# Kernel tuning notes

Measured on AMD Instinct MI355X. Metric: run time of the kernel, lower is better.

## Reference

```python
import jax
import jax.numpy as jnp
from jax import lax
import numpy as np

SLIDING_WINDOW_LEN = 192
EPS = 1e-6


def setup_inputs() -> dict:
    key = jax.random.key(0)
    X = jax.random.normal(key, (8, 8, 257, 2000), dtype=jnp.float32)
    return {"X": X, "ref_channel": 0}


def _forgetting_normalization(XrMag):
    # XrMag: [B, 1, F, T] magnitude of reference channel
    alpha = (SLIDING_WINDOW_LEN - 1) / (SLIDING_WINDOW_LEN + 1)
    # mean over frequency, keepdim -> [B, 1, 1, T]
    XrMM = XrMag.mean(axis=2, keepdims=True)
    T = XrMM.shape[-1]
    t = jnp.arange(T, dtype=XrMM.dtype)
    # original: alpha_this = min((t-1)/(t+1), alpha) for t < L, else alpha;
    # since (t-1)/(t+1) >= alpha for t >= L, a single minimum is exact.
    a = jnp.minimum((t - 1.0) / (t + 1.0), alpha)  # [T]

    x_seq = jnp.moveaxis(XrMM, -1, 0)  # [T, B, 1, 1]
    mu0 = jnp.zeros_like(x_seq[0])

    def step(mu, inp):
        a_t, x_t = inp
        mu = a_t * mu + (1.0 - a_t) * x_t
        return mu, mu

    _, mus = lax.scan(step, mu0, (a, x_seq))  # [T, B, 1, 1]
    return jnp.moveaxis(mus, 0, -1)  # [B, 1, 1, T]


def reference(X, ref_channel):
    # X: [B, C, F, T] (real stand-in for complex); ref_channel: python int
    Xr = X[:, ref_channel:ref_channel + 1]  # [B, 1, F, T]
    XrMag = jnp.abs(Xr)
    # original detaches XrMM (.detach().cpu()) -> stop_gradient
    XrMM = lax.stop_gradient(_forgetting_normalization(XrMag)) + EPS  # [B,1,1,T]
    X_norm = X / XrMM  # broadcast over C, F
    return X_norm
```

## Files before the change

kernel.cpp:

```cpp
#include <hip/hip_runtime.h>

#define B_N 8
#define C_N 8
#define F_N 257
#define T_N 2000
#define TQ_N (T_N / 4)
#define EPSF 1e-6f

#define FCH 32
#define FPC 9
#define PER_B (C_N * F_N * TQ_N)

#define NBPB   256
#define NTHR_C 256
#define CSTRIDE (NBPB * NTHR_C)
#define CDT     (CSTRIDE % TQ_N)

typedef float f32x4 __attribute__((ext_vector_type(4)));

__global__ __launch_bounds__(512) void partial_mean_kernel(
    const float* __restrict__ X, const int* __restrict__ ref_ch,
    f32x4* __restrict__ part4 )
{
    const int b = blockIdx.x, c = blockIdx.y, tid = threadIdx.x;
    if (tid >= TQ_N) return;

    const int rc = ref_ch[0];
    const f32x4* Xb4 =
        (const f32x4*)(X + ((size_t)(b * C_N + rc)) * (size_t)F_N * T_N);

    const int f0 = c * FPC;
    const int f1 = (f0 + FPC < F_N) ? (f0 + FPC) : F_N;

    f32x4 acc = {0.f, 0.f, 0.f, 0.f};
    for (int f = f0; f < f1; ++f) {
        f32x4 v = Xb4[f * TQ_N + tid];
        acc.x += fabsf(v.x); acc.y += fabsf(v.y);
        acc.z += fabsf(v.z); acc.w += fabsf(v.w);
    }
    part4[(b * FCH + c) * TQ_N + tid] = acc;
}

__global__ __launch_bounds__(512) void scan_kernel(
    const f32x4* __restrict__ part4,
    f32x4* __restrict__ inv4 )
{
    __shared__ float s_mean[T_N];
    __shared__ float s_wA[8];
    __shared__ float s_wB[8];
    const float ALPHA = (float)(191.0 / 193.0);
    const int b = blockIdx.x, tid = threadIdx.x;

    if (tid < TQ_N) {
        f32x4 s = {0.f, 0.f, 0.f, 0.f};
        #pragma unroll
        for (int c = 0; c < FCH; ++c)
            s += part4[(b * FCH + c) * TQ_N + tid];
        const int t = tid * 4;
        const float inv_f = 1.f / (float)F_N;
        s_mean[t + 0] = s.x * inv_f; s_mean[t + 1] = s.y * inv_f;
        s_mean[t + 2] = s.z * inv_f; s_mean[t + 3] = s.w * inv_f;
    }
    __syncthreads();

    float A = 1.f, Bv = 0.f;
    const int tbase = tid * 4;
    #pragma unroll
    for (int k = 0; k < 4; ++k) {
        const int t = tbase + k;
        if (t < T_N) {
            const float tf = (float)t;
            const float a = fminf((tf - 1.f) / (tf + 1.f), ALPHA);
            Bv = a * Bv + (1.f - a) * s_mean[t];
            A  = a * A;
        }
    }
    const int lane = tid & 63;
    #pragma unroll
    for (int d = 1; d < 64; d <<= 1) {
        const float pA = __shfl_up(A, d);
        const float pB = __shfl_up(Bv, d);
        if (lane >= d) { Bv = A * pB + Bv; A = A * pA; }
    }
    const int wid = tid >> 6;
    if (lane == 63) { s_wA[wid] = A; s_wB[wid] = Bv; }
    __syncthreads();
    if (tid == 0) {
        float cA = 1.f, cB = 0.f;
        #pragma unroll
        for (int w = 0; w < 8; ++w) {
            const float nA = s_wA[w] * cA;
            const float nB = s_wA[w] * cB + s_wB[w];
            s_wA[w] = cA; s_wB[w] = cB;
            cA = nA; cB = nB;
        }
    }
    __syncthreads();
    float eA = __shfl_up(A, 1);
    float eB = __shfl_up(Bv, 1);
    if (lane == 0) { eA = 1.f; eB = 0.f; }
    float mu = eA * s_wB[wid] + eB;

    if (tid < TQ_N) {
        f32x4 r;
        #pragma unroll
        for (int k = 0; k < 4; ++k) {
            const int t = tbase + k;
            const float tf = (float)t;
            const float a = fminf((tf - 1.f) / (tf + 1.f), ALPHA);
            mu = a * mu + (1.f - a) * s_mean[t];
            r[k] = 1.f / (mu + EPSF);
        }
        inv4[b * TQ_N + tid] = r;
    }
}

__global__ __launch_bounds__(NTHR_C) void norm_kernel(
    const f32x4* __restrict__ X4,
    const f32x4* __restrict__ inv4,
    f32x4* __restrict__ out4)
{
    const int b = blockIdx.y;
    const f32x4* Xb  = X4   + (size_t)b * PER_B;
    f32x4*       Ob  = out4 + (size_t)b * PER_B;
    const f32x4* ivb = inv4 + b * TQ_N;

    int i  = blockIdx.x * NTHR_C + threadIdx.x;
    int tq = i % TQ_N;
    for (; i < PER_B; i += CSTRIDE) {
        Ob[i] = Xb[i] * ivb[tq];
        tq += CDT; if (tq >= TQ_N) tq -= TQ_N;
    }
}

extern "C" void kernel_launch(void* const* d_in, const int* in_sizes, int n_in,
                              void* d_out, int out_size, void* d_ws, size_t ws_size,
                              hipStream_t stream) {
    const float* X  = (const float*)d_in[0];
    const int*   rc = (const int*)d_in[1];

    f32x4* inv  = (f32x4*)d_ws;
    f32x4* part = inv + B_N * TQ_N;

    dim3 gA(B_N, FCH);
    partial_mean_kernel<<<gA, 512, 0, stream>>>(X, rc, part);

    scan_kernel<<<B_N, 512, 0, stream>>>(part, inv);

    dim3 gC(NBPB, B_N);
    norm_kernel<<<gC, NTHR_C, 0, stream>>>((const f32x4*)X, inv, (f32x4*)d_out);
}
```

Before: 65.40 us.

## Fuse forgetting scan into normalization kernel and reduce means in one pass

```diff
diff --git a/kernel.cpp b/kernel.cpp
--- a/kernel.cpp
+++ b/kernel.cpp
@@ -6,72 +6,81 @@
 #define T_N 2000
 #define TQ_N (T_N / 4)
 #define EPSF 1e-6f
-
-#define FCH 32
-#define FPC 9
 #define PER_B (C_N * F_N * TQ_N)
-
-#define NBPB   256
-#define NTHR_C 256
-#define CSTRIDE (NBPB * NTHR_C)
-#define CDT     (CSTRIDE % TQ_N)
 
 typedef float f32x4 __attribute__((ext_vector_type(4)));
 
-__global__ __launch_bounds__(512) void partial_mean_kernel(
+__global__ __launch_bounds__(512) void mean_kernel(
     const float* __restrict__ X, const int* __restrict__ ref_ch,
-    f32x4* __restrict__ part4 )
+    f32x4* __restrict__ mean4 )
 {
-    const int b = blockIdx.x, c = blockIdx.y, tid = threadIdx.x;
-    if (tid >= TQ_N) return;
+    __shared__ f32x4 s_red[512];
+    const int b   = blockIdx.x;
+    const int qb  = blockIdx.y * 16;
+    const int tid = threadIdx.x;
+    const int fi  = tid >> 4;
+    const int qi  = tid & 15;
+    const int q   = qb + qi;
 
     const int rc = ref_ch[0];
     const f32x4* Xb4 =
         (const f32x4*)(X + ((size_t)(b * C_N + rc)) * (size_t)F_N * T_N);
 
-    const int f0 = c * FPC;
-    const int f1 = (f0 + FPC < F_N) ? (f0 + FPC) : F_N;
-
     f32x4 acc = {0.f, 0.f, 0.f, 0.f};
-    for (int f = f0; f < f1; ++f) {
-        f32x4 v = Xb4[f * TQ_N + tid];
-        acc.x += fabsf(v.x); acc.y += fabsf(v.y);
-        acc.z += fabsf(v.z); acc.w += fabsf(v.w);
+    if (q < TQ_N) {
+        for (int f = fi; f < F_N; f += 32) {
+            f32x4 v = Xb4[f * TQ_N + q];
+            acc.x += fabsf(v.x); acc.y += fabsf(v.y);
+            acc.z += fabsf(v.z); acc.w += fabsf(v.w);
+        }
     }
-    part4[(b * FCH + c) * TQ_N + tid] = acc;
+    s_red[tid] = acc;
+    __syncthreads();
+    #pragma unroll
+    for (int s = 256; s >= 16; s >>= 1) {
+        if (tid < s) s_red[tid] += s_red[tid + s];
+        __syncthreads();
+    }
+    if (tid < 16) {
+        const int qq = qb + tid;
+        if (qq < TQ_N)
+            mean4[b * TQ_N + qq] = s_red[tid] * (1.f / (float)F_N);
+    }
 }
 
-__global__ __launch_bounds__(512) void scan_kernel(
-    const f32x4* __restrict__ part4,
-    f32x4* __restrict__ inv4 )
+__global__ __launch_bounds__(512) void norm_scan_kernel(
+    const f32x4* __restrict__ X4,
+    const f32x4* __restrict__ mean4,
+    f32x4* __restrict__ out4)
 {
-    __shared__ float s_mean[T_N];
+    __shared__ f32x4 s_inv4[TQ_N];
     __shared__ float s_wA[8];
     __shared__ float s_wB[8];
     const float ALPHA = (float)(191.0 / 193.0);
-    const int b = blockIdx.x, tid = threadIdx.x;
 
-    if (tid < TQ_N) {
-        f32x4 s = {0.f, 0.f, 0.f, 0.f};
-        #pragma unroll
-        for (int c = 0; c < FCH; ++c)
-            s += part4[(b * FCH + c) * TQ_N + tid];
-        const int t = tid * 4;
-        const float inv_f = 1.f / (float)F_N;
-        s_mean[t + 0] = s.x * inv_f; s_mean[t + 1] = s.y * inv_f;
-        s_mean[t + 2] = s.z * inv_f; s_mean[t + 3] = s.w * inv_f;
-    }
-    __syncthreads();
+    const int b   = blockIdx.y;
+    const int tid = threadIdx.x;
+
+    const f32x4* Xb = X4   + (size_t)b * PER_B;
+    f32x4*       Ob = out4 + (size_t)b * PER_B;
+
+    const int  i     = blockIdx.x * 512 + tid;
+    const bool valid = (i < PER_B);
+    f32x4 x = {0.f, 0.f, 0.f, 0.f};
+    int   tq = 0;
+    if (valid) { x = Xb[i]; tq = i % TQ_N; }
+
+    f32x4 m = {0.f, 0.f, 0.f, 0.f};
+    if (tid < TQ_N) m = mean4[b * TQ_N + tid];
 
     float A = 1.f, Bv = 0.f;
     const int tbase = tid * 4;
-    #pragma unroll
-    for (int k = 0; k < 4; ++k) {
-        const int t = tbase + k;
-        if (t < T_N) {
-            const float tf = (float)t;
-            const float a = fminf((tf - 1.f) / (tf + 1.f), ALPHA);
-            Bv = a * Bv + (1.f - a) * s_mean[t];
+    if (tid < TQ_N) {
+        #pragma unroll
+        for (int k = 0; k < 4; ++k) {
+            const float tf = (float)(tbase + k);
+            const float a  = fminf((tf - 1.f) / (tf + 1.f), ALPHA);
+            Bv = a * Bv + (1.f - a) * m[k];
             A  = a * A;
         }
     }
@@ -105,32 +114,16 @@
         f32x4 r;
         #pragma unroll
         for (int k = 0; k < 4; ++k) {
-            const int t = tbase + k;
-            const float tf = (float)t;
-            const float a = fminf((tf - 1.f) / (tf + 1.f), ALPHA);
-            mu = a * mu + (1.f - a) * s_mean[t];
+            const float tf = (float)(tbase + k);
+            const float a  = fminf((tf - 1.f) / (tf + 1.f), ALPHA);
+            mu = a * mu + (1.f - a) * m[k];
             r[k] = 1.f / (mu + EPSF);
         }
-        inv4[b * TQ_N + tid] = r;
+        s_inv4[tid] = r;
     }
-}
+    __syncthreads();
 
-__global__ __launch_bounds__(NTHR_C) void norm_kernel(
-    const f32x4* __restrict__ X4,
-    const f32x4* __restrict__ inv4,
-    f32x4* __restrict__ out4)
-{
-    const int b = blockIdx.y;
-    const f32x4* Xb  = X4   + (size_t)b * PER_B;
-    f32x4*       Ob  = out4 + (size_t)b * PER_B;
-    const f32x4* ivb = inv4 + b * TQ_N;
-
-    int i  = blockIdx.x * NTHR_C + threadIdx.x;
-    int tq = i % TQ_N;
-    for (; i < PER_B; i += CSTRIDE) {
-        Ob[i] = Xb[i] * ivb[tq];
-        tq += CDT; if (tq >= TQ_N) tq -= TQ_N;
-    }
+    if (valid) Ob[i] = x * s_inv4[tq];
 }
 
 extern "C" void kernel_launch(void* const* d_in, const int* in_sizes, int n_in,
@@ -139,14 +132,12 @@
     const float* X  = (const float*)d_in[0];
     const int*   rc = (const int*)d_in[1];
 
-    f32x4* inv  = (f32x4*)d_ws;
-    f32x4* part = inv + B_N * TQ_N;
+    f32x4* mean = (f32x4*)d_ws;
 
-    dim3 gA(B_N, FCH);
-    partial_mean_kernel<<<gA, 512, 0, stream>>>(X, rc, part);
+    dim3 gA(B_N, 32);
+    mean_kernel<<<gA, 512, 0, stream>>>(X, rc, mean);
 
-    scan_kernel<<<B_N, 512, 0, stream>>>(part, inv);
-
-    dim3 gC(NBPB, B_N);
-    norm_kernel<<<gC, NTHR_C, 0, stream>>>((const f32x4*)X, inv, (f32x4*)d_out);
+    dim3 gC((PER_B + 511) / 512, B_N);
+    norm_scan_kernel<<<gC, 512, 0, stream>>>(
+        (const f32x4*)X, (const f32x4*)mean, (f32x4*)d_out);
 }
```

New measurement: 63.22 us. -3.3%, faster.
